# Kernel tuning notes

Hardware: AMD Instinct MI355X
Metric: run time of the kernel (lower is better)

Reference implementation:

```python
import jax, jax.numpy as jnp
import numpy as np


def setup_inputs() -> dict:
    key = jax.random.key(0)
    k1, k2, k3, k4, k5 = jax.random.split(key, 5)
    B, S, H, F, E = 2, 512, 1024, 3584, 8
    scale_in = 1.0 / np.sqrt(H)
    scale_ff = 1.0 / np.sqrt(F)
    return {
        "hidden_states": jax.random.normal(k1, (B, S, H), dtype=jnp.float32),
        "gate_w": jax.random.normal(k2, (E, H), dtype=jnp.float32) * scale_in,
        "w1": jax.random.normal(k3, (E, F, H), dtype=jnp.float32) * scale_in,
        "w2": jax.random.normal(k4, (E, H, F), dtype=jnp.float32) * scale_ff,
        "w3": jax.random.normal(k5, (E, F, H), dtype=jnp.float32) * scale_in,
    }


TOP_K = 2


def reference(hidden_states, gate_w, w1, w2, w3):
    B, S, H = hidden_states.shape
    E = gate_w.shape[0]
    x = hidden_states.reshape(B * S, H)  # [T, H]
    T = x.shape[0]

    # Router: softmax in fp32, top-2 selection, renormalize selected weights.
    router_logits = x @ gate_w.T  # [T, E]
    probs = jax.nn.softmax(router_logits.astype(jnp.float32), axis=-1)
    top_vals, top_idx = jax.lax.top_k(probs, TOP_K)  # [T, K]
    top_vals = top_vals / jnp.sum(top_vals, axis=-1, keepdims=True)
    top_vals = top_vals.astype(x.dtype)

    # Dense routing-weight matrix [T, E]: weight if selected else 0
    # (equivalent to the one-hot expert_mask + index_add combine).
    dense_w = jnp.zeros((T, E), dtype=x.dtype).at[
        jnp.arange(T)[:, None], top_idx
    ].add(top_vals)

    # Expert SwiGLU MLPs, batched over the expert axis.
    h1 = jnp.einsum("th,efh->etf", x, w1)  # [E, T, F]
    h3 = jnp.einsum("th,efh->etf", x, w3)  # [E, T, F]
    y = jnp.einsum("etf,ehf->eth", jax.nn.silu(h1) * h3, w2)  # [E, T, H]

    # Weighted combine across experts.
    out = jnp.einsum("eth,te->th", y, dense_w)  # [T, H]
    return out.reshape(B, S, H), router_logits
```

## Files before the change

### kernel.cpp

```cpp
#include <hip/hip_runtime.h>
#include <hip/hip_bf16.h>

typedef __bf16 v8bf __attribute__((ext_vector_type(8)));
typedef __bf16 v4bf __attribute__((ext_vector_type(4)));
typedef float  f32x4 __attribute__((ext_vector_type(4)));
typedef unsigned int u32;

#define NTOK 1024
#define HDIM 1024
#define FDIM 3584
#define NEXP 8
#define NPAIR 2048
#define MAXT 32
#define KSPLIT2 4
#define KPER2 (FDIM / KSPLIT2)

#define OFF_COUNTS   0
#define OFF_OFFSETS  64
#define OFF_NT1      128
#define OFF_T1E      192
#define OFF_T1M      320
#define OFF_TOKIDX   2048
#define OFF_TOKWT    (2048 + 4*NPAIR)
#define OFF_PAIRTOK  (OFF_TOKWT + 4*NPAIR)
#define OFF_PAIRWT   (OFF_PAIRTOK + 4*NPAIR)
#define OFF_SLOTOF   (OFF_PAIRWT + 4*NPAIR)
#define OFF_XB       65536
#define OFF_ACT      (OFF_XB + 2ull*NTOK*HDIM)
#define OFF_Y        (OFF_ACT + 2ull*NPAIR*FDIM)
#define YSTRIDE      ((size_t)NPAIR * HDIM)

static __device__ inline v4bf cvt4(float4 f) {
    v4bf r;
    r[0] = (__bf16)f.x; r[1] = (__bf16)f.y; r[2] = (__bf16)f.z; r[3] = (__bf16)f.w;
    return r;
}

static __device__ inline v8bf pack8(f32x4 lo, f32x4 hi) {
    v8bf r;
    r[0] = (__bf16)lo[0]; r[1] = (__bf16)lo[1]; r[2] = (__bf16)lo[2]; r[3] = (__bf16)lo[3];
    r[4] = (__bf16)hi[0]; r[5] = (__bf16)hi[1]; r[6] = (__bf16)hi[2]; r[7] = (__bf16)hi[3];
    return r;
}

#define FENCE() asm volatile("" ::: "memory")
#define BARRIER() do { FENCE(); __builtin_amdgcn_s_barrier(); FENCE(); } while (0)
#define WAITVM0() asm volatile("s_waitcnt vmcnt(0)" ::: "memory")
#define WAITLGKM0() asm volatile("s_waitcnt lgkmcnt(0)" ::: "memory")

#define DMA16(SRC, DST) \
    __builtin_amdgcn_global_load_lds((const __attribute__((address_space(1))) u32*)(SRC), \
                                     (__attribute__((address_space(3))) u32*)(DST), 16, 0, 0)

__global__ __launch_bounds__(256) void moe_cvtx(const float* __restrict__ x,
                                                __bf16* __restrict__ xb)
{
    const size_t i = ((size_t)blockIdx.x * 256 + threadIdx.x) * 4;
    float4 v = *(const float4*)(x + i);
    *(v4bf*)(xb + i) = cvt4(v);
}

__global__ __launch_bounds__(256) void moe_router(
    const float* __restrict__ x, const float* __restrict__ gw,
    float* __restrict__ logits, int* __restrict__ counts,
    int* __restrict__ tok_idx, float* __restrict__ tok_wt)
{
    const int lane = threadIdx.x & 63;
    const int wv = threadIdx.x >> 6;
    const int t = blockIdx.x * 4 + wv;
    const float* xr = x + (size_t)t * HDIM;

    float acc[NEXP];
#pragma unroll
    for (int e = 0; e < NEXP; ++e) acc[e] = 0.f;
#pragma unroll
    for (int j = 0; j < 4; ++j) {
        int h = lane * 4 + j * 256;
        float4 xv = *(const float4*)(xr + h);
#pragma unroll
        for (int e = 0; e < NEXP; ++e) {
            float4 g = *(const float4*)(gw + e * HDIM + h);
            acc[e] += xv.x * g.x + xv.y * g.y + xv.z * g.z + xv.w * g.w;
        }
    }
#pragma unroll
    for (int e = 0; e < NEXP; ++e) {
#pragma unroll
        for (int s = 32; s > 0; s >>= 1) acc[e] += __shfl_xor(acc[e], s);
    }
    if (lane == 0) {
#pragma unroll
        for (int e = 0; e < NEXP; ++e) logits[t * NEXP + e] = acc[e];
        int i0 = 0;
#pragma unroll
        for (int e = 1; e < NEXP; ++e) if (acc[e] > acc[i0]) i0 = e;
        int i1 = (i0 == 0) ? 1 : 0;
#pragma unroll
        for (int e = 0; e < NEXP; ++e) if (e != i0 && acc[e] > acc[i1]) i1 = e;
        float w0 = 1.f / (1.f + expf(acc[i1] - acc[i0]));
        float w1 = 1.f - w0;
        tok_idx[2 * t] = i0; tok_idx[2 * t + 1] = i1;
        tok_wt[2 * t] = w0;  tok_wt[2 * t + 1] = w1;
        atomicAdd(&counts[i0], 1);
        atomicAdd(&counts[i1], 1);
    }
}

__global__ void moe_scatter(const int* __restrict__ counts, const int* __restrict__ tok_idx,
                            const float* __restrict__ tok_wt, int* __restrict__ offsets,
                            int* __restrict__ pair_token, float* __restrict__ pair_wt,
                            int* __restrict__ slot_of,
                            int* __restrict__ t1e, int* __restrict__ t1m, int* __restrict__ nt1)
{
    __shared__ int cur[NEXP];
    const int tid = threadIdx.x;
    if (tid == 0) {
        int run = 0, n1 = 0;
        for (int e = 0; e < NEXP; ++e) {
            offsets[e] = run; cur[e] = run;
            for (int m0 = 0; m0 < counts[e]; m0 += 128) { t1e[n1] = e; t1m[n1] = m0; ++n1; }
            run += counts[e];
        }
        *nt1 = n1;
    }
    __syncthreads();
    for (int p = tid; p < 2 * NTOK; p += blockDim.x) {
        int e = tok_idx[p];
        int s = atomicAdd(&cur[e], 1);
        pair_token[s] = p >> 1;
        pair_wt[s] = tok_wt[p];
        slot_of[p] = s;
    }
}

__global__ __launch_bounds__(256, 4) void moe_gemm1(
    const __bf16* __restrict__ xb, const float* __restrict__ w1g,
    const float* __restrict__ w3g, const int* __restrict__ counts,
    const int* __restrict__ offsets, const int* __restrict__ pair_token,
    const int* __restrict__ t1e, const int* __restrict__ t1m,
    const int* __restrict__ nt1,
    __bf16* __restrict__ act)
{
    const int ty = blockIdx.y;
    if (ty >= *nt1) return;
    const int e = t1e[ty];
    const int m0 = t1m[ty];
    const int Me = counts[e];
    const int rows = min(128, Me - m0);
    const int slot0 = offsets[e] + m0;
    const int n0 = blockIdx.x * 64;

    __shared__ __align__(16) __bf16 As[128 * 32];
    __shared__ __align__(16) float  B1s[64 * 32];
    __shared__ __align__(16) float  B3s[64 * 32];

    const int tid = threadIdx.x;
    const int lane = tid & 63;
    const int wv = tid >> 6;
    const int ln4 = lane >> 4;
    const int lr = lane & 15;
    const int wm = (wv >> 1) * 64;
    const int wn = (wv & 1) * 32;

    f32x4 acc1[4][2], acc3[4][2];
#pragma unroll
    for (int i = 0; i < 4; ++i)
#pragma unroll
        for (int j = 0; j < 2; ++j) {
            acc1[i][j] = (f32x4){0.f, 0.f, 0.f, 0.f};
            acc3[i][j] = (f32x4){0.f, 0.f, 0.f, 0.f};
        }

    const char* asrc[2];
#pragma unroll
    for (int i = 0; i < 2; ++i) {
        int c = i * 256 + tid;
        int r = c >> 2;
        int rr = (r < rows) ? r : 0;
        int sj = (c & 3) ^ ((r >> 1) & 3);
        asrc[i] = (const char*)(xb + (size_t)pair_token[slot0 + rr] * HDIM) + sj * 16;
    }
    const char* bsrc[2];
#pragma unroll
    for (int i = 0; i < 2; ++i) {
        int c = i * 256 + tid;
        int r = c >> 3;
        int sj = (c & 7) ^ (r & 7);
        bsrc[i] = (const char*)(w1g + ((size_t)e * FDIM + n0 + r) * HDIM) + sj * 16;
    }
    const ptrdiff_t d31b = (const char*)w3g - (const char*)w1g;

#define DMA_ALL1(K0) do { _Pragma("unroll") \
    for (int i = 0; i < 2; ++i) { \
        DMA16(asrc[i] + (size_t)(K0) * 64,         (char*)As  + (i * 256 + wv * 64) * 16); \
        DMA16(bsrc[i] + (size_t)(K0) * 128,        (char*)B1s + (i * 256 + wv * 64) * 16); \
        DMA16(bsrc[i] + d31b + (size_t)(K0) * 128, (char*)B3s + (i * 256 + wv * 64) * 16); \
    } } while (0)

    int aoff[4];
#pragma unroll
    for (int i = 0; i < 4; ++i) {
        int row = wm + i * 16 + lr;
        aoff[i] = row * 64 + ((ln4 ^ ((row >> 1) & 3)) * 16);
    }
    int blo[2], bhi[2];
#pragma unroll
    for (int i = 0; i < 2; ++i) {
        int row = wn + i * 16 + lr;
        blo[i] = row * 128 + (((ln4 * 2) ^ (row & 7)) * 16);
        bhi[i] = row * 128 + (((ln4 * 2 + 1) ^ (row & 7)) * 16);
    }

#define CMP1() do { \
    v8bf af[4], b1f[2], b3f[2]; \
    _Pragma("unroll") \
    for (int i = 0; i < 4; ++i) af[i] = *(const v8bf*)((const char*)As + aoff[i]); \
    _Pragma("unroll") \
    for (int i = 0; i < 2; ++i) { \
        b1f[i] = pack8(*(const f32x4*)((const char*)B1s + blo[i]), \
                       *(const f32x4*)((const char*)B1s + bhi[i])); \
        b3f[i] = pack8(*(const f32x4*)((const char*)B3s + blo[i]), \
                       *(const f32x4*)((const char*)B3s + bhi[i])); } \
    _Pragma("unroll") \
    for (int mi = 0; mi < 4; ++mi) { _Pragma("unroll") \
        for (int ni = 0; ni < 2; ++ni) { \
            acc1[mi][ni] = __builtin_amdgcn_mfma_f32_16x16x32_bf16(af[mi], b1f[ni], acc1[mi][ni], 0, 0, 0); \
            acc3[mi][ni] = __builtin_amdgcn_mfma_f32_16x16x32_bf16(af[mi], b3f[ni], acc3[mi][ni], 0, 0, 0); } } \
    } while (0)

    DMA_ALL1(0);
    for (int ks = 0; ks < HDIM / 32; ++ks) {
        WAITVM0();
        BARRIER();
        CMP1();
        WAITLGKM0();
        BARRIER();
        if (ks + 1 < HDIM / 32) DMA_ALL1(ks + 1);
    }
#undef DMA_ALL1
#undef CMP1

    const int rj = ln4 * 4;
#pragma unroll
    for (int mi = 0; mi < 4; ++mi) {
#pragma unroll
        for (int j = 0; j < 4; ++j) {
            int rm = wm + mi * 16 + rj + j;
            if (rm < rows) {
                size_t rowoff = (size_t)(slot0 + rm) * FDIM + n0 + wn;
#pragma unroll
                for (int ni = 0; ni < 2; ++ni) {
                    float h1 = acc1[mi][ni][j];
                    float h3 = acc3[mi][ni][j];
                    float sv = (h1 / (1.f + __expf(-h1))) * h3;
                    act[rowoff + ni * 16 + lr] = (__bf16)sv;
                }
            }
        }
    }
}

__global__ __launch_bounds__(256, 4) void moe_gemm2(
    const __bf16* __restrict__ act, const float* __restrict__ w2g,
    const int* __restrict__ counts, const int* __restrict__ offsets,
    const int* __restrict__ t1e, const int* __restrict__ t1m,
    const int* __restrict__ nt1,
    float* __restrict__ y)
{
    const int ty = blockIdx.y;
    if (ty >= *nt1) return;
    const int e = t1e[ty];
    const int m0 = t1m[ty];
    const int Me = counts[e];
    const int rows = min(128, Me - m0);
    const int slot0 = offsets[e] + m0;
    const int n0 = blockIdx.x * 128;
    const int kz = blockIdx.z;
    float* yout = y + (size_t)kz * YSTRIDE;
    const size_t kbase = (size_t)kz * KPER2;

    __shared__ __align__(16) __bf16 As[128 * 32];
    __shared__ __align__(16) float  Bs[128 * 32];

    const int tid = threadIdx.x;
    const int lane = tid & 63;
    const int wv = tid >> 6;
    const int ln4 = lane >> 4;
    const int lr = lane & 15;
    const int wm = (wv >> 1) * 64;
    const int wn = (wv & 1) * 64;

    f32x4 acc[4][4];
#pragma unroll
    for (int i = 0; i < 4; ++i)
#pragma unroll
        for (int j = 0; j < 4; ++j) acc[i][j] = (f32x4){0.f, 0.f, 0.f, 0.f};

    const char* asrc[2];
#pragma unroll
    for (int i = 0; i < 2; ++i) {
        int c = i * 256 + tid;
        int r = c >> 2;
        int rr = (r < rows) ? r : 0;
        int sj = (c & 3) ^ ((r >> 1) & 3);
        asrc[i] = (const char*)(act + (size_t)(slot0 + rr) * FDIM + kbase) + sj * 16;
    }
    const char* bsrc[4];
#pragma unroll
    for (int i = 0; i < 4; ++i) {
        int c = i * 256 + tid;
        int r = c >> 3;
        int sj = (c & 7) ^ (r & 7);
        bsrc[i] = (const char*)(w2g + ((size_t)e * HDIM + n0 + r) * FDIM + kbase) + sj * 16;
    }

#define DMA_ALL2(K0) do { \
    _Pragma("unroll") \
    for (int i = 0; i < 2; ++i) \
        DMA16(asrc[i] + (size_t)(K0) * 64, (char*)As + (i * 256 + wv * 64) * 16); \
    _Pragma("unroll") \
    for (int i = 0; i < 4; ++i) \
        DMA16(bsrc[i] + (size_t)(K0) * 128, (char*)Bs + (i * 256 + wv * 64) * 16); \
    } while (0)

    int aoff[4];
#pragma unroll
    for (int i = 0; i < 4; ++i) {
        int row = wm + i * 16 + lr;
        aoff[i] = row * 64 + ((ln4 ^ ((row >> 1) & 3)) * 16);
    }
    int blo[4], bhi[4];
#pragma unroll
    for (int i = 0; i < 4; ++i) {
        int row = wn + i * 16 + lr;
        blo[i] = row * 128 + (((ln4 * 2) ^ (row & 7)) * 16);
        bhi[i] = row * 128 + (((ln4 * 2 + 1) ^ (row & 7)) * 16);
    }

#define CMP2() do { \
    v8bf af[4], bf[4]; \
    _Pragma("unroll") \
    for (int i = 0; i < 4; ++i) af[i] = *(const v8bf*)((const char*)As + aoff[i]); \
    _Pragma("unroll") \
    for (int i = 0; i < 4; ++i) \
        bf[i] = pack8(*(const f32x4*)((const char*)Bs + blo[i]), \
                      *(const f32x4*)((const char*)Bs + bhi[i])); \
    _Pragma("unroll") \
    for (int mi = 0; mi < 4; ++mi) { _Pragma("unroll") \
        for (int ni = 0; ni < 4; ++ni) \
            acc[mi][ni] = __builtin_amdgcn_mfma_f32_16x16x32_bf16(af[mi], bf[ni], acc[mi][ni], 0, 0, 0); } \
    } while (0)

    DMA_ALL2(0);
    for (int ks = 0; ks < KPER2 / 32; ++ks) {
        WAITVM0();
        BARRIER();
        CMP2();
        WAITLGKM0();
        BARRIER();
        if (ks + 1 < KPER2 / 32) DMA_ALL2(ks + 1);
    }
#undef DMA_ALL2
#undef CMP2

    const int rj = ln4 * 4;
#pragma unroll
    for (int mi = 0; mi < 4; ++mi) {
#pragma unroll
        for (int j = 0; j < 4; ++j) {
            int rm = wm + mi * 16 + rj + j;
            if (rm < rows) {
                size_t rowoff = (size_t)(slot0 + rm) * HDIM + n0 + wn;
#pragma unroll
                for (int ni = 0; ni < 4; ++ni)
                    yout[rowoff + ni * 16 + lr] = acc[mi][ni][j];
            }
        }
    }
}

__global__ __launch_bounds__(256) void moe_combine(
    const float* __restrict__ y, const int* __restrict__ slot_of,
    const float* __restrict__ pair_wt, float* __restrict__ out)
{
    const int t = blockIdx.x;
    const int tid = threadIdx.x;
    const int s0 = slot_of[2 * t];
    const int s1 = slot_of[2 * t + 1];
    const float w0 = pair_wt[s0];
    const float w1 = pair_wt[s1];
    float4 a = {0.f, 0.f, 0.f, 0.f}, b = {0.f, 0.f, 0.f, 0.f};
#pragma unroll
    for (int k = 0; k < KSPLIT2; ++k) {
        const float4 ak = *(const float4*)(y + k * YSTRIDE + (size_t)s0 * HDIM + tid * 4);
        const float4 bk = *(const float4*)(y + k * YSTRIDE + (size_t)s1 * HDIM + tid * 4);
        a.x += ak.x; a.y += ak.y; a.z += ak.z; a.w += ak.w;
        b.x += bk.x; b.y += bk.y; b.z += bk.z; b.w += bk.w;
    }
    float4 o;
    o.x = w0 * a.x + w1 * b.x;
    o.y = w0 * a.y + w1 * b.y;
    o.z = w0 * a.z + w1 * b.z;
    o.w = w0 * a.w + w1 * b.w;
    *(float4*)(out + (size_t)t * HDIM + tid * 4) = o;
}

extern "C" void kernel_launch(void* const* d_in, const int* in_sizes, int n_in,
                              void* d_out, int out_size, void* d_ws, size_t ws_size,
                              hipStream_t stream) {
    const float* x   = (const float*)d_in[0];
    const float* gw  = (const float*)d_in[1];
    const float* w1  = (const float*)d_in[2];
    const float* w2  = (const float*)d_in[3];
    const float* w3  = (const float*)d_in[4];

    float* out    = (float*)d_out;
    float* logits = out + (size_t)NTOK * HDIM;

    char* ws = (char*)d_ws;
    int*    counts     = (int*)(ws + OFF_COUNTS);
    int*    offsets    = (int*)(ws + OFF_OFFSETS);
    int*    nt1        = (int*)(ws + OFF_NT1);
    int*    t1e        = (int*)(ws + OFF_T1E);
    int*    t1m        = (int*)(ws + OFF_T1M);
    int*    tok_idx    = (int*)(ws + OFF_TOKIDX);
    float*  tok_wt     = (float*)(ws + OFF_TOKWT);
    int*    pair_token = (int*)(ws + OFF_PAIRTOK);
    float*  pair_wt    = (float*)(ws + OFF_PAIRWT);
    int*    slot_of    = (int*)(ws + OFF_SLOTOF);
    __bf16* xb         = (__bf16*)(ws + OFF_XB);
    __bf16* act        = (__bf16*)(ws + OFF_ACT);
    float*  yb         = (float*)(ws + OFF_Y);

    hipMemsetAsync(counts, 0, 64, stream);

    moe_cvtx<<<dim3(NTOK * HDIM / 1024), dim3(256), 0, stream>>>(x, xb);
    moe_router<<<dim3(NTOK / 4), dim3(256), 0, stream>>>(x, gw, logits, counts, tok_idx, tok_wt);
    moe_scatter<<<dim3(1), dim3(256), 0, stream>>>(counts, tok_idx, tok_wt, offsets,
                                                   pair_token, pair_wt, slot_of,
                                                   t1e, t1m, nt1);
    moe_gemm1<<<dim3(FDIM / 64, MAXT), dim3(256), 0, stream>>>(
        xb, w1, w3, counts, offsets, pair_token, t1e, t1m, nt1, act);
    moe_gemm2<<<dim3(HDIM / 128, MAXT, KSPLIT2), dim3(256), 0, stream>>>(
        act, w2, counts, offsets, t1e, t1m, nt1, yb);
    moe_combine<<<dim3(NTOK), dim3(256), 0, stream>>>(yb, slot_of, pair_wt, out);
}
```

Measured before the change: 220.4 us.

## Stream expert weights straight to registers and double-buffer token tiles in LDS

Both expert GEMMs now load the fp32 weight fragments directly from global memory into registers and pack them to bf16 there, instead of staging them through LDS. Only the bf16 activation tile goes through LDS, now double-buffered with a 64-wide K step so one barrier per stage suffices. The second GEMM also moves to 64-column tiles with a split-K of 2 and a lower occupancy hint. This is meant to cut LDS traffic and barrier stalls on the weight-bandwidth-bound path. The cost is global-load latency exposed in the MFMA loop and weight rows loaded twice by the two waves that share a column slice.

```diff
diff --git a/kernel.cpp b/kernel.cpp
--- a/kernel.cpp
+++ b/kernel.cpp
@@ -12,7 +12,7 @@
 #define NEXP 8
 #define NPAIR 2048
 #define MAXT 32
-#define KSPLIT2 4
+#define KSPLIT2 2
 #define KPER2 (FDIM / KSPLIT2)
 
 #define OFF_COUNTS   0
@@ -44,7 +44,6 @@
 }
 
 #define FENCE() asm volatile("" ::: "memory")
-#define BARRIER() do { FENCE(); __builtin_amdgcn_s_barrier(); FENCE(); } while (0)
 #define WAITVM0() asm volatile("s_waitcnt vmcnt(0)" ::: "memory")
 #define WAITLGKM0() asm volatile("s_waitcnt lgkmcnt(0)" ::: "memory")
 
@@ -133,7 +132,7 @@
     }
 }
 
-__global__ __launch_bounds__(256, 4) void moe_gemm1(
+__global__ __launch_bounds__(256, 2) void moe_gemm1(
     const __bf16* __restrict__ xb, const float* __restrict__ w1g,
     const float* __restrict__ w3g, const int* __restrict__ counts,
     const int* __restrict__ offsets, const int* __restrict__ pair_token,
@@ -150,9 +149,7 @@
     const int slot0 = offsets[e] + m0;
     const int n0 = blockIdx.x * 64;
 
-    __shared__ __align__(16) __bf16 As[128 * 32];
-    __shared__ __align__(16) float  B1s[64 * 32];
-    __shared__ __align__(16) float  B3s[64 * 32];
+    __shared__ __align__(16) __bf16 As[2][128 * 64];
 
     const int tid = threadIdx.x;
     const int lane = tid & 63;
@@ -171,74 +168,81 @@
             acc3[i][j] = (f32x4){0.f, 0.f, 0.f, 0.f};
         }
 
-    const char* asrc[2];
-#pragma unroll
-    for (int i = 0; i < 2; ++i) {
-        int c = i * 256 + tid;
-        int r = c >> 2;
-        int rr = (r < rows) ? r : 0;
-        int sj = (c & 3) ^ ((r >> 1) & 3);
-        asrc[i] = (const char*)(xb + (size_t)pair_token[slot0 + rr] * HDIM) + sj * 16;
-    }
-    const char* bsrc[2];
-#pragma unroll
-    for (int i = 0; i < 2; ++i) {
+    const char* asrc[4];
+#pragma unroll
+    for (int i = 0; i < 4; ++i) {
         int c = i * 256 + tid;
         int r = c >> 3;
+        int rr = (r < rows) ? r : 0;
         int sj = (c & 7) ^ (r & 7);
-        bsrc[i] = (const char*)(w1g + ((size_t)e * FDIM + n0 + r) * HDIM) + sj * 16;
-    }
-    const ptrdiff_t d31b = (const char*)w3g - (const char*)w1g;
-
-#define DMA_ALL1(K0) do { _Pragma("unroll") \
-    for (int i = 0; i < 2; ++i) { \
-        DMA16(asrc[i] + (size_t)(K0) * 64,         (char*)As  + (i * 256 + wv * 64) * 16); \
-        DMA16(bsrc[i] + (size_t)(K0) * 128,        (char*)B1s + (i * 256 + wv * 64) * 16); \
-        DMA16(bsrc[i] + d31b + (size_t)(K0) * 128, (char*)B3s + (i * 256 + wv * 64) * 16); \
-    } } while (0)
-
-    int aoff[4];
-#pragma unroll
-    for (int i = 0; i < 4; ++i) {
-        int row = wm + i * 16 + lr;
-        aoff[i] = row * 64 + ((ln4 ^ ((row >> 1) & 3)) * 16);
-    }
-    int blo[2], bhi[2];
-#pragma unroll
-    for (int i = 0; i < 2; ++i) {
-        int row = wn + i * 16 + lr;
-        blo[i] = row * 128 + (((ln4 * 2) ^ (row & 7)) * 16);
-        bhi[i] = row * 128 + (((ln4 * 2 + 1) ^ (row & 7)) * 16);
-    }
-
-#define CMP1() do { \
-    v8bf af[4], b1f[2], b3f[2]; \
-    _Pragma("unroll") \
-    for (int i = 0; i < 4; ++i) af[i] = *(const v8bf*)((const char*)As + aoff[i]); \
-    _Pragma("unroll") \
-    for (int i = 0; i < 2; ++i) { \
-        b1f[i] = pack8(*(const f32x4*)((const char*)B1s + blo[i]), \
-                       *(const f32x4*)((const char*)B1s + bhi[i])); \
-        b3f[i] = pack8(*(const f32x4*)((const char*)B3s + blo[i]), \
-                       *(const f32x4*)((const char*)B3s + bhi[i])); } \
-    _Pragma("unroll") \
-    for (int mi = 0; mi < 4; ++mi) { _Pragma("unroll") \
-        for (int ni = 0; ni < 2; ++ni) { \
-            acc1[mi][ni] = __builtin_amdgcn_mfma_f32_16x16x32_bf16(af[mi], b1f[ni], acc1[mi][ni], 0, 0, 0); \
-            acc3[mi][ni] = __builtin_amdgcn_mfma_f32_16x16x32_bf16(af[mi], b3f[ni], acc3[mi][ni], 0, 0, 0); } } \
+        asrc[i] = (const char*)(xb + (size_t)pair_token[slot0 + rr] * HDIM) + sj * 16;
+    }
+
+    const float* b1p[2];
+    const float* b3p[2];
+#pragma unroll
+    for (int ni = 0; ni < 2; ++ni) {
+        size_t row = (size_t)e * FDIM + n0 + wn + ni * 16 + lr;
+        b1p[ni] = w1g + row * HDIM + ln4 * 8;
+        b3p[ni] = w3g + row * HDIM + ln4 * 8;
+    }
+
+    int aoff[4][2];
+#pragma unroll
+    for (int mi = 0; mi < 4; ++mi) {
+#pragma unroll
+        for (int kh = 0; kh < 2; ++kh) {
+            int row = wm + mi * 16 + lr;
+            aoff[mi][kh] = row * 128 + ((kh * 64 + ln4 * 16) ^ ((row & 7) << 4));
+        }
+    }
+
+#define DMA_A1(BUF, K0) do { _Pragma("unroll") \
+    for (int i = 0; i < 4; ++i) \
+        DMA16(asrc[i] + (size_t)(K0) * 2, (char*)&As[BUF][0] + (i * 256 + wv * 64) * 16); \
     } while (0)
 
-    DMA_ALL1(0);
-    for (int ks = 0; ks < HDIM / 32; ++ks) {
-        WAITVM0();
-        BARRIER();
-        CMP1();
-        WAITLGKM0();
-        BARRIER();
-        if (ks + 1 < HDIM / 32) DMA_ALL1(ks + 1);
-    }
-#undef DMA_ALL1
-#undef CMP1
+    DMA_A1(0, 0);
+    WAITVM0();
+    FENCE(); __builtin_amdgcn_s_barrier(); FENCE();
+
+    int buf = 0;
+    for (int ks = 0; ks < HDIM / 64; ++ks) {
+        if (ks + 1 < HDIM / 64) DMA_A1(buf ^ 1, (ks + 1) * 64);
+#pragma unroll
+        for (int kh = 0; kh < 2; ++kh) {
+            const int k0 = ks * 64 + kh * 32;
+            v8bf b1f[2], b3f[2];
+#pragma unroll
+            for (int ni = 0; ni < 2; ++ni) {
+                f32x4 lo1 = *(const f32x4*)(b1p[ni] + k0);
+                f32x4 hi1 = *(const f32x4*)(b1p[ni] + k0 + 4);
+                f32x4 lo3 = *(const f32x4*)(b3p[ni] + k0);
+                f32x4 hi3 = *(const f32x4*)(b3p[ni] + k0 + 4);
+                b1f[ni] = pack8(lo1, hi1);
+                b3f[ni] = pack8(lo3, hi3);
+            }
+            v8bf af[4];
+#pragma unroll
+            for (int mi = 0; mi < 4; ++mi)
+                af[mi] = *(const v8bf*)((const char*)&As[buf][0] + aoff[mi][kh]);
+#pragma unroll
+            for (int mi = 0; mi < 4; ++mi) {
+#pragma unroll
+                for (int ni = 0; ni < 2; ++ni) {
+                    acc1[mi][ni] = __builtin_amdgcn_mfma_f32_16x16x32_bf16(af[mi], b1f[ni], acc1[mi][ni], 0, 0, 0);
+                    acc3[mi][ni] = __builtin_amdgcn_mfma_f32_16x16x32_bf16(af[mi], b3f[ni], acc3[mi][ni], 0, 0, 0);
+                }
+            }
+        }
+        if (ks + 1 < HDIM / 64) {
+            WAITVM0();
+            WAITLGKM0();
+            FENCE(); __builtin_amdgcn_s_barrier(); FENCE();
+            buf ^= 1;
+        }
+    }
+#undef DMA_A1
 
     const int rj = ln4 * 4;
 #pragma unroll
@@ -260,7 +264,7 @@
     }
 }
 
-__global__ __launch_bounds__(256, 4) void moe_gemm2(
+__global__ __launch_bounds__(256, 2) void moe_gemm2(
     const __bf16* __restrict__ act, const float* __restrict__ w2g,
     const int* __restrict__ counts, const int* __restrict__ offsets,
     const int* __restrict__ t1e, const int* __restrict__ t1m,
@@ -274,13 +278,12 @@
     const int Me = counts[e];
     const int rows = min(128, Me - m0);
     const int slot0 = offsets[e] + m0;
-    const int n0 = blockIdx.x * 128;
+    const int n0 = blockIdx.x * 64;
     const int kz = blockIdx.z;
     float* yout = y + (size_t)kz * YSTRIDE;
     const size_t kbase = (size_t)kz * KPER2;
 
-    __shared__ __align__(16) __bf16 As[128 * 32];
-    __shared__ __align__(16) float  Bs[128 * 32];
+    __shared__ __align__(16) __bf16 As[2][128 * 64];
 
     const int tid = threadIdx.x;
     const int lane = tid & 63;
@@ -288,80 +291,82 @@
     const int ln4 = lane >> 4;
     const int lr = lane & 15;
     const int wm = (wv >> 1) * 64;
-    const int wn = (wv & 1) * 64;
-
-    f32x4 acc[4][4];
+    const int wn = (wv & 1) * 32;
+
+    f32x4 acc[4][2];
 #pragma unroll
     for (int i = 0; i < 4; ++i)
 #pragma unroll
-        for (int j = 0; j < 4; ++j) acc[i][j] = (f32x4){0.f, 0.f, 0.f, 0.f};
-
-    const char* asrc[2];
-#pragma unroll
-    for (int i = 0; i < 2; ++i) {
-        int c = i * 256 + tid;
-        int r = c >> 2;
-        int rr = (r < rows) ? r : 0;
-        int sj = (c & 3) ^ ((r >> 1) & 3);
-        asrc[i] = (const char*)(act + (size_t)(slot0 + rr) * FDIM + kbase) + sj * 16;
-    }
-    const char* bsrc[4];
+        for (int j = 0; j < 2; ++j) acc[i][j] = (f32x4){0.f, 0.f, 0.f, 0.f};
+
+    const char* asrc[4];
 #pragma unroll
     for (int i = 0; i < 4; ++i) {
         int c = i * 256 + tid;
         int r = c >> 3;
+        int rr = (r < rows) ? r : 0;
         int sj = (c & 7) ^ (r & 7);
-        bsrc[i] = (const char*)(w2g + ((size_t)e * HDIM + n0 + r) * FDIM + kbase) + sj * 16;
-    }
-
-#define DMA_ALL2(K0) do { \
-    _Pragma("unroll") \
-    for (int i = 0; i < 2; ++i) \
-        DMA16(asrc[i] + (size_t)(K0) * 64, (char*)As + (i * 256 + wv * 64) * 16); \
-    _Pragma("unroll") \
+        asrc[i] = (const char*)(act + (size_t)(slot0 + rr) * FDIM + kbase) + sj * 16;
+    }
+
+    const float* bp[2];
+#pragma unroll
+    for (int ni = 0; ni < 2; ++ni) {
+        size_t row = (size_t)e * HDIM + n0 + wn + ni * 16 + lr;
+        bp[ni] = w2g + row * FDIM + kbase + ln4 * 8;
+    }
+
+    int aoff[4][2];
+#pragma unroll
+    for (int mi = 0; mi < 4; ++mi) {
+#pragma unroll
+        for (int kh = 0; kh < 2; ++kh) {
+            int row = wm + mi * 16 + lr;
+            aoff[mi][kh] = row * 128 + ((kh * 64 + ln4 * 16) ^ ((row & 7) << 4));
+        }
+    }
+
+#define DMA_A2(BUF, K0) do { _Pragma("unroll") \
     for (int i = 0; i < 4; ++i) \
-        DMA16(bsrc[i] + (size_t)(K0) * 128, (char*)Bs + (i * 256 + wv * 64) * 16); \
+        DMA16(asrc[i] + (size_t)(K0) * 2, (char*)&As[BUF][0] + (i * 256 + wv * 64) * 16); \
     } while (0)
 
-    int aoff[4];
-#pragma unroll
-    for (int i = 0; i < 4; ++i) {
-        int row = wm + i * 16 + lr;
-        aoff[i] = row * 64 + ((ln4 ^ ((row >> 1) & 3)) * 16);
-    }
-    int blo[4], bhi[4];
-#pragma unroll
-    for (int i = 0; i < 4; ++i) {
-        int row = wn + i * 16 + lr;
-        blo[i] = row * 128 + (((ln4 * 2) ^ (row & 7)) * 16);
-        bhi[i] = row * 128 + (((ln4 * 2 + 1) ^ (row & 7)) * 16);
-    }
-
-#define CMP2() do { \
-    v8bf af[4], bf[4]; \
-    _Pragma("unroll") \
-    for (int i = 0; i < 4; ++i) af[i] = *(const v8bf*)((const char*)As + aoff[i]); \
-    _Pragma("unroll") \
-    for (int i = 0; i < 4; ++i) \
-        bf[i] = pack8(*(const f32x4*)((const char*)Bs + blo[i]), \
-                      *(const f32x4*)((const char*)Bs + bhi[i])); \
-    _Pragma("unroll") \
-    for (int mi = 0; mi < 4; ++mi) { _Pragma("unroll") \
-        for (int ni = 0; ni < 4; ++ni) \
-            acc[mi][ni] = __builtin_amdgcn_mfma_f32_16x16x32_bf16(af[mi], bf[ni], acc[mi][ni], 0, 0, 0); } \
-    } while (0)
-
-    DMA_ALL2(0);
-    for (int ks = 0; ks < KPER2 / 32; ++ks) {
-        WAITVM0();
-        BARRIER();
-        CMP2();
-        WAITLGKM0();
-        BARRIER();
-        if (ks + 1 < KPER2 / 32) DMA_ALL2(ks + 1);
-    }
-#undef DMA_ALL2
-#undef CMP2
+    DMA_A2(0, 0);
+    WAITVM0();
+    FENCE(); __builtin_amdgcn_s_barrier(); FENCE();
+
+    int buf = 0;
+    for (int ks = 0; ks < KPER2 / 64; ++ks) {
+        if (ks + 1 < KPER2 / 64) DMA_A2(buf ^ 1, (ks + 1) * 64);
+#pragma unroll
+        for (int kh = 0; kh < 2; ++kh) {
+            const int k0 = ks * 64 + kh * 32;
+            v8bf bf[2];
+#pragma unroll
+            for (int ni = 0; ni < 2; ++ni) {
+                f32x4 lo = *(const f32x4*)(bp[ni] + k0);
+                f32x4 hi = *(const f32x4*)(bp[ni] + k0 + 4);
+                bf[ni] = pack8(lo, hi);
+            }
+            v8bf af[4];
+#pragma unroll
+            for (int mi = 0; mi < 4; ++mi)
+                af[mi] = *(const v8bf*)((const char*)&As[buf][0] + aoff[mi][kh]);
+#pragma unroll
+            for (int mi = 0; mi < 4; ++mi) {
+#pragma unroll
+                for (int ni = 0; ni < 2; ++ni)
+                    acc[mi][ni] = __builtin_amdgcn_mfma_f32_16x16x32_bf16(af[mi], bf[ni], acc[mi][ni], 0, 0, 0);
+            }
+        }
+        if (ks + 1 < KPER2 / 64) {
+            WAITVM0();
+            WAITLGKM0();
+            FENCE(); __builtin_amdgcn_s_barrier(); FENCE();
+            buf ^= 1;
+        }
+    }
+#undef DMA_A2
 
     const int rj = ln4 * 4;
 #pragma unroll
@@ -372,7 +377,7 @@
             if (rm < rows) {
                 size_t rowoff = (size_t)(slot0 + rm) * HDIM + n0 + wn;
 #pragma unroll
-                for (int ni = 0; ni < 4; ++ni)
+                for (int ni = 0; ni < 2; ++ni)
                     yout[rowoff + ni * 16 + lr] = acc[mi][ni][j];
             }
         }
@@ -441,7 +446,7 @@
                                                    t1e, t1m, nt1);
     moe_gemm1<<<dim3(FDIM / 64, MAXT), dim3(256), 0, stream>>>(
         xb, w1, w3, counts, offsets, pair_token, t1e, t1m, nt1, act);
-    moe_gemm2<<<dim3(HDIM / 128, MAXT, KSPLIT2), dim3(256), 0, stream>>>(
+    moe_gemm2<<<dim3(HDIM / 64, MAXT, KSPLIT2), dim3(256), 0, stream>>>(
         act, w2, counts, offsets, t1e, t1m, nt1, yb);
     moe_combine<<<dim3(NTOK), dim3(256), 0, stream>>>(yb, slot_of, pair_wt, out);
 }
```

Result: slower. 341.9 us (+55.1%).
